# Kernel optimization log

Measured on AMD Instinct MI355X. Metric: run time of the kernel, lower is better.

The kernel has to match this reference:

```python
import jax, jax.numpy as jnp
import numpy as np

D = 6       # stalk_dimension
RANK = 2    # low-rank factor


def setup_inputs() -> dict:
    key = jax.random.key(0)
    k = jax.random.split(key, 8)
    N, E, NNZ, F = 100000, 20000, 1000000, 64
    x = jax.random.normal(k[0], (N * D, F), dtype=jnp.float32)
    e = jax.random.normal(k[1], (E * D, F), dtype=jnp.float32)
    W = jax.random.normal(k[2], (2 * F, 2 * D * RANK + D), dtype=jnp.float32) * 0.05
    b = jnp.zeros((2 * D * RANK + D,), dtype=jnp.float32)
    row = jax.random.randint(k[3], (NNZ,), 0, N, dtype=jnp.int64)
    col = jax.random.randint(k[4], (NNZ,), 0, E, dtype=jnp.int64)
    hyperedge_index = jnp.stack([row, col], axis=0)
    node_types = jax.random.randint(k[5], (N,), 0, 4, dtype=jnp.int64)
    hyperedge_types = jax.random.randint(k[6], (E,), 0, 6, dtype=jnp.int64)
    return {"x": x, "e": e, "W": W, "b": b,
            "hyperedge_index": hyperedge_index,
            "node_types": node_types, "hyperedge_types": hyperedge_types}


def reference(x, e, W, b, hyperedge_index, node_types, hyperedge_types):
    d, r = D, RANK
    num_nodes = x.shape[0] // d
    num_edges = e.shape[0] // d
    # mean over stalk copies -> [N, F], [E, F]
    x = x.reshape(num_nodes, d, x.shape[-1]).mean(axis=1)
    e = e.reshape(num_edges, d, e.shape[-1]).mean(axis=1)
    row, col = hyperedge_index[0], hyperedge_index[1]
    # var1 he-features: identity; local_concat sheaf predictor
    h = jnp.concatenate([x[row], e[col]], axis=-1)          # [nnz, 2F]
    h_sheaf = jax.nn.sigmoid(h @ W + b)                     # [nnz, 2*d*r + d]
    A = h_sheaf[:, : d * r].reshape(-1, d, r)
    B = h_sheaf[:, d * r: 2 * d * r].reshape(-1, d, r)
    C = h_sheaf[:, 2 * d * r:]                              # [nnz, d]
    maps = jnp.einsum('nir,njr->nij', A, B)                 # A @ B^T
    maps = maps + C[:, :, None] * jnp.eye(d, dtype=maps.dtype)  # diag_embed(C)
    h_attrs = maps.reshape(-1)                              # [nnz*d*d]
    # sparse COO index construction
    dr = jnp.arange(d, dtype=row.dtype)
    off_nodes = jnp.repeat(dr, d)                           # repeat_interleave
    off_edges = jnp.tile(dr, d)                             # repeat
    idx0 = (d * row[:, None] + off_nodes[None, :]).reshape(-1)
    idx1 = (d * col[:, None] + off_edges[None, :]).reshape(-1)
    h_sheaf_index = jnp.stack([idx0, idx1], axis=0)         # [2, nnz*d*d]
    return (h_sheaf_index, h_attrs)
```

## Files before the change

kernel.cpp:

```cpp
#include <hip/hip_runtime.h>
#include <hip/hip_bf16.h>

#define DD 6
#define FF 64
#define NS 30
#define TS16 32
#define UPB 32

typedef float fx4 __attribute__((ext_vector_type(4)));

__device__ __forceinline__ float fast_sigmoid(float v) {
    return __builtin_amdgcn_rcpf(1.0f + __expf(-v));
}
__device__ __forceinline__ void nt_store4(float* p, float a, float b, float c, float d) {
    fx4 v = {a, b, c, d};
    __builtin_nontemporal_store(v, (fx4*)p);
}

__global__ __launch_bounds__(256) void precompute_kernel(
    const float* __restrict__ x, const float* __restrict__ e,
    const float* __restrict__ W, const float* __restrict__ bias,
    __hip_bfloat16* __restrict__ xW, __hip_bfloat16* __restrict__ eW,
    int N, int E, int nbN)
{
    __shared__ float means[UPB][68];
    bool isNode = (int)blockIdx.x < nbN;
    int ucount  = isNode ? N : E;
    int ubase   = (isNode ? blockIdx.x : (blockIdx.x - nbN)) * UPB;
    const float* src = isNode ? x : e;
    const float* Wp  = W + (isNode ? 0 : FF * NS);
    __hip_bfloat16* dst = isNode ? xW : eW;

    int tid = threadIdx.x, wid = tid >> 6, lane = tid & 63;

    #pragma unroll
    for (int i = 0; i < 8; ++i) {
        int s = wid * 8 + i;
        int u = ubase + s;
        float m = 0.f;
        if (u < ucount) {
            const float* p = src + (size_t)u * (DD * FF) + lane;
            #pragma unroll
            for (int d = 0; d < DD; ++d) m += p[d * FF];
        }
        means[s][lane] = m * (1.0f / 6.0f);
    }
    __syncthreads();

    int j30 = lane & 31;
    bool jval = j30 < NS;
    int j = jval ? j30 : 0;
    float wreg[FF];
    #pragma unroll
    for (int f = 0; f < FF; ++f) wreg[f] = Wp[f * NS + j];
    float bj = isNode ? bias[j] : 0.f;

    #pragma unroll
    for (int t = 0; t < 4; ++t) {
        int sl = wid * 8 + 2 * t + (lane >> 5);
        int u  = ubase + sl;
        const fx4* mp4 = (const fx4*)(&means[sl][0]);
        float o = bj;
        #pragma unroll
        for (int q = 0; q < 16; ++q) {
            fx4 m4 = mp4[q];
            o = fmaf(m4.x, wreg[4 * q + 0], o);
            o = fmaf(m4.y, wreg[4 * q + 1], o);
            o = fmaf(m4.z, wreg[4 * q + 2], o);
            o = fmaf(m4.w, wreg[4 * q + 3], o);
        }
        if (jval && u < ucount)
            dst[(size_t)u * TS16 + j30] = __float2bfloat16(o);
    }
}

__global__ __launch_bounds__(256) void fused_kernel(
    const int* __restrict__ rows, const int* __restrict__ cols,
    const __hip_bfloat16* __restrict__ xW, const __hip_bfloat16* __restrict__ eW,
    float* __restrict__ out_idx0, float* __restrict__ out_idx1,
    float* __restrict__ out_attr, int nnz)
{
    __shared__ float mlds[4][32 * 37];
    __shared__ int rlds[256], clds[256];
    int tid  = threadIdx.x, wid = tid >> 6, lane = tid & 63;
    int bb   = blockIdx.x * 256;
    int k    = bb + tid;
    bool act = k < nnz;

    float mp[36];
    if (act) {
        int r = rows[k];
        int c = cols[k];
        rlds[tid] = r; clds[tid] = c;
        const uint4* xp = (const uint4*)(xW + (size_t)r * TS16);
        const uint4* ep = (const uint4*)(eW + (size_t)c * TS16);
        uint4 xa0 = xp[0], xa1 = xp[1], xa2 = xp[2], xa3 = xp[3];
        uint4 ea0 = ep[0], ea1 = ep[1], ea2 = ep[2], ea3 = ep[3];
        uint wx[16] = {xa0.x, xa0.y, xa0.z, xa0.w, xa1.x, xa1.y, xa1.z, xa1.w,
                       xa2.x, xa2.y, xa2.z, xa2.w, xa3.x, xa3.y, xa3.z, xa3.w};
        uint we[16] = {ea0.x, ea0.y, ea0.z, ea0.w, ea1.x, ea1.y, ea1.z, ea1.w,
                       ea2.x, ea2.y, ea2.z, ea2.w, ea3.x, ea3.y, ea3.z, ea3.w};
        float s[NS];
        #pragma unroll
        for (int j2 = 0; j2 < NS; ++j2) {
            uint ux = (j2 & 1) ? (wx[j2 >> 1] & 0xffff0000u) : (wx[j2 >> 1] << 16);
            uint ue = (j2 & 1) ? (we[j2 >> 1] & 0xffff0000u) : (we[j2 >> 1] << 16);
            s[j2] = fast_sigmoid(__uint_as_float(ux) + __uint_as_float(ue));
        }
        #pragma unroll
        for (int i = 0; i < DD; ++i) {
            float a0 = s[i * 2], a1 = s[i * 2 + 1];
            #pragma unroll
            for (int jj = 0; jj < DD; ++jj) {
                float v = fmaf(a0, s[12 + jj * 2], a1 * s[13 + jj * 2]);
                if (i == jj) v += s[24 + i];
                mp[i * 6 + jj] = v;
            }
        }
    }

    float* wl = mlds[wid];
    int wbase = bb + wid * 64;
    #pragma unroll
    for (int h = 0; h < 2; ++h) {
        if (h) __syncthreads();
        if (act && (lane >> 5) == h) {
            float* ml = wl + (lane & 31) * 37;
            #pragma unroll
            for (int m = 0; m < 36; ++m) ml[m] = mp[m];
        }
        __syncthreads();
        int b2  = wbase + h * 32;
        int cnt = nnz - b2; if (cnt > 32) cnt = 32;
        if (cnt > 0) {
            int tot = cnt * 36;
            size_t ob = (size_t)b2 * 36;
            float* ga = out_attr + ob;
            float* g0 = out_idx0 + ob;
            float* g1 = out_idx1 + ob;
            int lb = wid * 64 + h * 32;
            for (int g = lane * 4; g < tot; g += 256) {
                int l = g / 36;
                int m = g - l * 36;
                const float* mlp = wl + l * 37 + m;
                int rr = rlds[lb + l], cc = clds[lb + l];
                float v0[4], v1[4];
                #pragma unroll
                for (int i = 0; i < 4; ++i) {
                    int mm = m + i;
                    int m6 = mm / 6;
                    v0[i] = (float)(6 * rr + m6);
                    v1[i] = (float)(6 * cc + (mm - m6 * 6));
                }
                nt_store4(ga + g, mlp[0], mlp[1], mlp[2], mlp[3]);
                nt_store4(g0 + g, v0[0], v0[1], v0[2], v0[3]);
                nt_store4(g1 + g, v1[0], v1[1], v1[2], v1[3]);
            }
        }
    }
}

__global__ __launch_bounds__(256) void sheaf_kernel(
    const int* __restrict__ rows, const int* __restrict__ cols,
    const __hip_bfloat16* __restrict__ xW, const __hip_bfloat16* __restrict__ eW,
    float* __restrict__ out_attr, int nnz)
{
    __shared__ float mlds[4][32 * 37];
    int tid = threadIdx.x, wid = tid >> 6, lane = tid & 63;
    int bb  = blockIdx.x * 256;
    int k   = bb + tid;
    bool act = k < nnz;
    float mp[36];
    if (act) {
        int r = rows[k];
        int c = cols[k];
        const uint4* xp = (const uint4*)(xW + (size_t)r * TS16);
        const uint4* ep = (const uint4*)(eW + (size_t)c * TS16);
        uint4 xa0 = xp[0], xa1 = xp[1], xa2 = xp[2], xa3 = xp[3];
        uint4 ea0 = ep[0], ea1 = ep[1], ea2 = ep[2], ea3 = ep[3];
        uint wx[16] = {xa0.x, xa0.y, xa0.z, xa0.w, xa1.x, xa1.y, xa1.z, xa1.w,
                       xa2.x, xa2.y, xa2.z, xa2.w, xa3.x, xa3.y, xa3.z, xa3.w};
        uint we[16] = {ea0.x, ea0.y, ea0.z, ea0.w, ea1.x, ea1.y, ea1.z, ea1.w,
                       ea2.x, ea2.y, ea2.z, ea2.w, ea3.x, ea3.y, ea3.z, ea3.w};
        float s[NS];
        #pragma unroll
        for (int j2 = 0; j2 < NS; ++j2) {
            uint ux = (j2 & 1) ? (wx[j2 >> 1] & 0xffff0000u) : (wx[j2 >> 1] << 16);
            uint ue = (j2 & 1) ? (we[j2 >> 1] & 0xffff0000u) : (we[j2 >> 1] << 16);
            s[j2] = fast_sigmoid(__uint_as_float(ux) + __uint_as_float(ue));
        }
        #pragma unroll
        for (int i = 0; i < DD; ++i) {
            float a0 = s[i * 2], a1 = s[i * 2 + 1];
            #pragma unroll
            for (int jj = 0; jj < DD; ++jj) {
                float v = fmaf(a0, s[12 + jj * 2], a1 * s[13 + jj * 2]);
                if (i == jj) v += s[24 + i];
                mp[i * 6 + jj] = v;
            }
        }
    }
    float* wl = mlds[wid];
    int wbase = bb + wid * 64;
    #pragma unroll
    for (int h = 0; h < 2; ++h) {
        if (h) __syncthreads();
        if (act && (lane >> 5) == h) {
            float* ml = wl + (lane & 31) * 37;
            #pragma unroll
            for (int m = 0; m < 36; ++m) ml[m] = mp[m];
        }
        __syncthreads();
        int b2  = wbase + h * 32;
        int cnt = nnz - b2; if (cnt > 32) cnt = 32;
        if (cnt > 0) {
            int tot = cnt * 36;
            float* gp = out_attr + (size_t)b2 * 36;
            for (int g = lane * 4; g < tot; g += 256) {
                int l = g / 36;
                int m = g - l * 36;
                const float* mlp = wl + l * 37 + m;
                nt_store4(gp + g, mlp[0], mlp[1], mlp[2], mlp[3]);
            }
        }
    }
}

__global__ __launch_bounds__(256) void idx_kernel(
    const int* __restrict__ rows, const int* __restrict__ cols,
    float* __restrict__ out_idx0, float* __restrict__ out_idx1, int tot)
{
    int g = (blockIdx.x * 256 + threadIdx.x) * 4;
    if (g >= tot) return;
    float v0[4], v1[4];
    #pragma unroll
    for (int i = 0; i < 4; ++i) {
        int gg = g + i;
        int l  = gg / 36;
        int m  = gg - l * 36;
        int m6 = m / 6;
        v0[i] = (float)(6 * rows[l] + m6);
        v1[i] = (float)(6 * cols[l] + (m - m6 * 6));
    }
    nt_store4(out_idx0 + g, v0[0], v0[1], v0[2], v0[3]);
    nt_store4(out_idx1 + g, v1[0], v1[1], v1[2], v1[3]);
}

extern "C" void kernel_launch(void* const* d_in, const int* in_sizes, int n_in,
                              void* d_out, int out_size, void* d_ws, size_t ws_size,
                              hipStream_t stream)
{
    const float* x = (const float*)d_in[0];
    const float* e = (const float*)d_in[1];
    const float* W = (const float*)d_in[2];
    const float* b = (const float*)d_in[3];
    const int* hidx = (const int*)d_in[4];

    int N   = in_sizes[0] / (DD * FF);
    int E   = in_sizes[1] / (DD * FF);
    int nnz = in_sizes[4] / 2;
    const int* rows = hidx;
    const int* cols = hidx + nnz;

    float* out = (float*)d_out;
    size_t M = (size_t)nnz * 36;
    float* out_idx0 = out;
    float* out_idx1 = out + M;
    float* out_attr = out + 2 * M;

    size_t tableBytes = ((size_t)N + (size_t)E) * TS16 * sizeof(__hip_bfloat16);
    bool haveWs = (ws_size >= tableBytes);
    __hip_bfloat16* xW = haveWs ? (__hip_bfloat16*)d_ws
                                : (__hip_bfloat16*)out_idx0;
    __hip_bfloat16* eW = xW + (size_t)N * TS16;

    int nbN = (N + UPB - 1) / UPB;
    int nbE = (E + UPB - 1) / UPB;
    precompute_kernel<<<nbN + nbE, 256, 0, stream>>>(x, e, W, b, xW, eW, N, E, nbN);

    int sBlocks = (nnz + 255) / 256;
    if (haveWs) {
        fused_kernel<<<sBlocks, 256, 0, stream>>>(rows, cols, xW, eW,
                                                  out_idx0, out_idx1, out_attr, nnz);
    } else {
        sheaf_kernel<<<sBlocks, 256, 0, stream>>>(rows, cols, xW, eW, out_attr, nnz);
        int tot = nnz * 36;
        int iBlocks = (tot / 4 + 255) / 256;
        idx_kernel<<<iBlocks, 256, 0, stream>>>(rows, cols, out_idx0, out_idx1, tot);
    }
}
```

Measured before the change: 130.9 us.

## Merge index generation into precompute launch to overlap with table build

The index-output writes no longer live in the fused sheaf kernel. They now run in the same grid as the node and edge projection precompute, with blocks split by blockIdx, and the sheaf kernel then writes only the attribute values. The aim is to hide the bandwidth-bound index stores behind the compute-light precompute phase instead of serialising them after it. In exchange, the sheaf kernel makes its own pass over the output, and the combined grid is much larger, so scheduling between the two block types may become unbalanced.

```diff
diff --git a/kernel.cpp b/kernel.cpp
--- a/kernel.cpp
+++ b/kernel.cpp
@@ -17,16 +17,17 @@
     __builtin_nontemporal_store(v, (fx4*)p);
 }
 
-__global__ __launch_bounds__(256) void precompute_kernel(
+
+__device__ __forceinline__ void precompute_body(
     const float* __restrict__ x, const float* __restrict__ e,
     const float* __restrict__ W, const float* __restrict__ bias,
     __hip_bfloat16* __restrict__ xW, __hip_bfloat16* __restrict__ eW,
-    int N, int E, int nbN)
+    int N, int E, int nbN, int blk)
 {
     __shared__ float means[UPB][68];
-    bool isNode = (int)blockIdx.x < nbN;
+    bool isNode = blk < nbN;
     int ucount  = isNode ? N : E;
-    int ubase   = (isNode ? blockIdx.x : (blockIdx.x - nbN)) * UPB;
+    int ubase   = (isNode ? blk : (blk - nbN)) * UPB;
     const float* src = isNode ? x : e;
     const float* Wp  = W + (isNode ? 0 : FF * NS);
     __hip_bfloat16* dst = isNode ? xW : eW;
@@ -74,89 +75,39 @@
     }
 }
 
-__global__ __launch_bounds__(256) void fused_kernel(
-    const int* __restrict__ rows, const int* __restrict__ cols,
-    const __hip_bfloat16* __restrict__ xW, const __hip_bfloat16* __restrict__ eW,
+__device__ __forceinline__ void idx_body(
+    const int* __restrict__ rows, const int* __restrict__ cols,
     float* __restrict__ out_idx0, float* __restrict__ out_idx1,
-    float* __restrict__ out_attr, int nnz)
-{
-    __shared__ float mlds[4][32 * 37];
-    __shared__ int rlds[256], clds[256];
-    int tid  = threadIdx.x, wid = tid >> 6, lane = tid & 63;
-    int bb   = blockIdx.x * 256;
-    int k    = bb + tid;
-    bool act = k < nnz;
-
-    float mp[36];
-    if (act) {
-        int r = rows[k];
-        int c = cols[k];
-        rlds[tid] = r; clds[tid] = c;
-        const uint4* xp = (const uint4*)(xW + (size_t)r * TS16);
-        const uint4* ep = (const uint4*)(eW + (size_t)c * TS16);
-        uint4 xa0 = xp[0], xa1 = xp[1], xa2 = xp[2], xa3 = xp[3];
-        uint4 ea0 = ep[0], ea1 = ep[1], ea2 = ep[2], ea3 = ep[3];
-        uint wx[16] = {xa0.x, xa0.y, xa0.z, xa0.w, xa1.x, xa1.y, xa1.z, xa1.w,
-                       xa2.x, xa2.y, xa2.z, xa2.w, xa3.x, xa3.y, xa3.z, xa3.w};
-        uint we[16] = {ea0.x, ea0.y, ea0.z, ea0.w, ea1.x, ea1.y, ea1.z, ea1.w,
-                       ea2.x, ea2.y, ea2.z, ea2.w, ea3.x, ea3.y, ea3.z, ea3.w};
-        float s[NS];
-        #pragma unroll
-        for (int j2 = 0; j2 < NS; ++j2) {
-            uint ux = (j2 & 1) ? (wx[j2 >> 1] & 0xffff0000u) : (wx[j2 >> 1] << 16);
-            uint ue = (j2 & 1) ? (we[j2 >> 1] & 0xffff0000u) : (we[j2 >> 1] << 16);
-            s[j2] = fast_sigmoid(__uint_as_float(ux) + __uint_as_float(ue));
-        }
-        #pragma unroll
-        for (int i = 0; i < DD; ++i) {
-            float a0 = s[i * 2], a1 = s[i * 2 + 1];
-            #pragma unroll
-            for (int jj = 0; jj < DD; ++jj) {
-                float v = fmaf(a0, s[12 + jj * 2], a1 * s[13 + jj * 2]);
-                if (i == jj) v += s[24 + i];
-                mp[i * 6 + jj] = v;
-            }
-        }
-    }
-
-    float* wl = mlds[wid];
-    int wbase = bb + wid * 64;
-    #pragma unroll
-    for (int h = 0; h < 2; ++h) {
-        if (h) __syncthreads();
-        if (act && (lane >> 5) == h) {
-            float* ml = wl + (lane & 31) * 37;
-            #pragma unroll
-            for (int m = 0; m < 36; ++m) ml[m] = mp[m];
-        }
-        __syncthreads();
-        int b2  = wbase + h * 32;
-        int cnt = nnz - b2; if (cnt > 32) cnt = 32;
-        if (cnt > 0) {
-            int tot = cnt * 36;
-            size_t ob = (size_t)b2 * 36;
-            float* ga = out_attr + ob;
-            float* g0 = out_idx0 + ob;
-            float* g1 = out_idx1 + ob;
-            int lb = wid * 64 + h * 32;
-            for (int g = lane * 4; g < tot; g += 256) {
-                int l = g / 36;
-                int m = g - l * 36;
-                const float* mlp = wl + l * 37 + m;
-                int rr = rlds[lb + l], cc = clds[lb + l];
-                float v0[4], v1[4];
-                #pragma unroll
-                for (int i = 0; i < 4; ++i) {
-                    int mm = m + i;
-                    int m6 = mm / 6;
-                    v0[i] = (float)(6 * rr + m6);
-                    v1[i] = (float)(6 * cc + (mm - m6 * 6));
-                }
-                nt_store4(ga + g, mlp[0], mlp[1], mlp[2], mlp[3]);
-                nt_store4(g0 + g, v0[0], v0[1], v0[2], v0[3]);
-                nt_store4(g1 + g, v1[0], v1[1], v1[2], v1[3]);
-            }
-        }
+    int tot, int ib)
+{
+    int g = (ib * 256 + (int)threadIdx.x) * 4;
+    if (g >= tot) return;
+    float v0[4], v1[4];
+    #pragma unroll
+    for (int i = 0; i < 4; ++i) {
+        int gg = g + i;
+        int l  = gg / 36;
+        int m  = gg - l * 36;
+        int m6 = m / 6;
+        v0[i] = (float)(6 * rows[l] + m6);
+        v1[i] = (float)(6 * cols[l] + (m - m6 * 6));
+    }
+    nt_store4(out_idx0 + g, v0[0], v0[1], v0[2], v0[3]);
+    nt_store4(out_idx1 + g, v1[0], v1[1], v1[2], v1[3]);
+}
+
+__global__ __launch_bounds__(256) void pre_idx_kernel(
+    const float* __restrict__ x, const float* __restrict__ e,
+    const float* __restrict__ W, const float* __restrict__ bias,
+    __hip_bfloat16* __restrict__ xW, __hip_bfloat16* __restrict__ eW,
+    const int* __restrict__ rows, const int* __restrict__ cols,
+    float* __restrict__ out_idx0, float* __restrict__ out_idx1,
+    int N, int E, int nbN, int nbPre, int nnz)
+{
+    if ((int)blockIdx.x < nbPre) {
+        precompute_body(x, e, W, bias, xW, eW, N, E, nbN, (int)blockIdx.x);
+    } else {
+        idx_body(rows, cols, out_idx0, out_idx1, nnz * 36, (int)blockIdx.x - nbPre);
     }
 }
 
@@ -230,20 +181,7 @@
     const int* __restrict__ rows, const int* __restrict__ cols,
     float* __restrict__ out_idx0, float* __restrict__ out_idx1, int tot)
 {
-    int g = (blockIdx.x * 256 + threadIdx.x) * 4;
-    if (g >= tot) return;
-    float v0[4], v1[4];
-    #pragma unroll
-    for (int i = 0; i < 4; ++i) {
-        int gg = g + i;
-        int l  = gg / 36;
-        int m  = gg - l * 36;
-        int m6 = m / 6;
-        v0[i] = (float)(6 * rows[l] + m6);
-        v1[i] = (float)(6 * cols[l] + (m - m6 * 6));
-    }
-    nt_store4(out_idx0 + g, v0[0], v0[1], v0[2], v0[3]);
-    nt_store4(out_idx1 + g, v1[0], v1[1], v1[2], v1[3]);
+    idx_body(rows, cols, out_idx0, out_idx1, tot, (int)blockIdx.x);
 }
 
 extern "C" void kernel_launch(void* const* d_in, const int* in_sizes, int n_in,
@@ -276,16 +214,21 @@
 
     int nbN = (N + UPB - 1) / UPB;
     int nbE = (E + UPB - 1) / UPB;
-    precompute_kernel<<<nbN + nbE, 256, 0, stream>>>(x, e, W, b, xW, eW, N, E, nbN);
-
+    int nbPre = nbN + nbE;
+    int tot = nnz * 36;
+    int iBlocks = (tot / 4 + 255) / 256;
     int sBlocks = (nnz + 255) / 256;
+
     if (haveWs) {
-        fused_kernel<<<sBlocks, 256, 0, stream>>>(rows, cols, xW, eW,
-                                                  out_idx0, out_idx1, out_attr, nnz);
+        pre_idx_kernel<<<nbPre + iBlocks, 256, 0, stream>>>(
+            x, e, W, b, xW, eW, rows, cols, out_idx0, out_idx1,
+            N, E, nbN, nbPre, nnz);
+        sheaf_kernel<<<sBlocks, 256, 0, stream>>>(rows, cols, xW, eW, out_attr, nnz);
     } else {
+        pre_idx_kernel<<<nbPre, 256, 0, stream>>>(
+            x, e, W, b, xW, eW, rows, cols, out_idx0, out_idx1,
+            N, E, nbN, nbPre, nnz);
         sheaf_kernel<<<sBlocks, 256, 0, stream>>>(rows, cols, xW, eW, out_attr, nnz);
-        int tot = nnz * 36;
-        int iBlocks = (tot / 4 + 255) / 256;
         idx_kernel<<<iBlocks, 256, 0, stream>>>(rows, cols, out_idx0, out_idx1, tot);
     }
 }
```

Result: faster. 123.1 us (-6.0%).
